# Optimization experiments

Measured on AMD Instinct MI355X. Metric: run time of the kernel, lower is better.

## Reference

```python
import jax, jax.numpy as jnp
import numpy as np

NFFT = 4096
BATCH = 2048
STAGES = 12  # log2(NFFT)


def _bitrev(n):
    bits = int(np.log2(n))
    idx = np.arange(n)
    rev = np.zeros(n, dtype=np.int64)
    for b in range(bits):
        rev |= ((idx >> b) & 1) << (bits - 1 - b)
    return rev


def setup_inputs() -> dict:
    key = jax.random.key(0)
    x = jax.random.normal(key, (BATCH, NFFT), dtype=jnp.float32)
    # bit-reversal permutation matrix, applied as x @ perm -> x[bitrev(k)]
    rev = _bitrev(NFFT)
    perm = np.zeros((NFFT, NFFT), dtype=np.float32)
    perm[rev, np.arange(NFFT)] = 1.0
    # per-stage butterfly weights (real/imag of twiddles), zero-padded to NFFT
    rconvs = np.zeros((STAGES, 2, NFFT), dtype=np.float32)
    iconvs = np.zeros((STAGES, 2, NFFT), dtype=np.float32)
    for i in range(STAGES):
        s = 2 ** (i + 1)
        h = 2 ** i
        th = 2.0 * np.pi * np.arange(h) / s  # twiddle w^j = exp(-i*th)
        c, sn = np.cos(th), np.sin(th)
        rconvs[i, 0, :s] = 1.0
        rconvs[i, 1, :s] = np.concatenate([c, -c])
        iconvs[i, 1, :s] = np.concatenate([-sn, sn])
    return {
        "x": x,
        "perm": jnp.asarray(perm),
        "rconvs": jnp.asarray(rconvs),
        "iconvs": jnp.asarray(iconvs),
    }


def _butterfly(x, w, h):
    # x: [B, M, 2h], w: [2, 2h]; equals the original diag-filter conv1d
    xt, xb = x[..., :h], x[..., h:]
    top = w[0, :h] * xt + w[1, :h] * xb
    bot = w[0, h:] * xt + w[1, h:] * xb
    return jnp.concatenate([top, bot], axis=-1)


def reference(x, perm, rconvs, iconvs):
    B = x.shape[0]
    rx = x @ perm  # bit-reversal reorder (dense matmul as in original)
    ix = jnp.zeros_like(rx)
    for i in range(STAGES):
        s = 2 ** (i + 1)
        h = 2 ** i
        rx = rx.reshape(B, -1, s)
        ix = ix.reshape(B, -1, s)
        rc = rconvs[i, :, :s]
        ic = iconvs[i, :, :s]
        nrx = _butterfly(rx, rc, h) - _butterfly(ix, ic, h)
        nix = _butterfly(ix, rc, h) + _butterfly(rx, ic, h)
        rx = nrx.reshape(B, -1)
        ix = nix.reshape(B, -1)
    return rx.reshape(B, 1, NFFT), ix.reshape(B, 1, NFFT)
```

## Files before the change

### kernel.cpp

```cpp
#include <hip/hip_runtime.h>


constexpr int NFFT  = 4096;
constexpr int BATCH = 2048;
constexpr int RS    = 18;

struct cplx { float re, im; };
__device__ __forceinline__ cplx cmul(cplx a, cplx b){ return {a.re*b.re - a.im*b.im, a.re*b.im + a.im*b.re}; }
__device__ __forceinline__ cplx cadd(cplx a, cplx b){ return {a.re+b.re, a.im+b.im}; }
__device__ __forceinline__ cplx csub(cplx a, cplx b){ return {a.re-b.re, a.im-b.im}; }
__device__ __forceinline__ cplx cnegi(cplx a){ return { a.im, -a.re }; }

__device__ __forceinline__ void dft4(cplx& a, cplx& b, cplx& c, cplx& d){
    cplx t0 = cadd(a,c), t1 = csub(a,c), t2 = cadd(b,d);
    cplx t3n = cnegi(csub(b,d));
    a = cadd(t0,t2);
    cplx nb = cadd(t1,t3n);
    c = csub(t0,t2);
    d = csub(t1,t3n);
    b = nb;
}

__device__ __forceinline__ constexpr int RIDX(int r){ return 4*(r&3) + (r>>2); }

__device__ __forceinline__ void dft16(cplx z[16]){
    dft4(z[0], z[4], z[8],  z[12]);
    dft4(z[1], z[5], z[9],  z[13]);
    dft4(z[2], z[6], z[10], z[14]);
    dft4(z[3], z[7], z[11], z[15]);
    constexpr float C1 = 0.92387953251128675613f;
    constexpr float S1 = 0.38268343236508977173f;
    constexpr float R2 = 0.70710678118654752440f;
    z[5]  = cmul(z[5],  { C1,-S1});
    z[6]  = cmul(z[6],  { R2,-R2});
    z[7]  = cmul(z[7],  { S1,-C1});
    z[9]  = cmul(z[9],  { R2,-R2});
    z[10] = cnegi(z[10]);
    z[11] = cmul(z[11], {-R2,-R2});
    z[13] = cmul(z[13], { S1,-C1});
    z[14] = cmul(z[14], {-R2,-R2});
    z[15] = cmul(z[15], {-C1, S1});
    dft4(z[0],  z[1],  z[2],  z[3]);
    dft4(z[4],  z[5],  z[6],  z[7]);
    dft4(z[8],  z[9],  z[10], z[11]);
    dft4(z[12], z[13], z[14], z[15]);
}

__device__ __forceinline__ void twiddle_all(cplx z[16], float rev){
    float ang = rev * 6.28318530717958647692f;
    float s = __sinf(ang), c = __cosf(ang);
    cplx w[16];
    w[0] = {1.0f, 0.0f};
    w[1] = {c, -s};
#pragma unroll
    for (int r = 2; r < 16; ++r) w[r] = cmul(w[r>>1], w[(r+1)>>1]);
#pragma unroll
    for (int r = 1; r < 16; ++r) z[RIDX(r)] = cmul(z[RIDX(r)], w[r]);
}

__global__ __launch_bounds__(256, 4)
void fft4096_r16(const float* __restrict__ x, float* __restrict__ out) {
    __shared__ float2 su[256 * RS];

    const int row = blockIdx.x;
    const int t   = threadIdx.x;
    const float* __restrict__ xr = x + (size_t)row * NFFT;

    cplx z[16];

#pragma unroll
    for (int n1 = 0; n1 < 16; ++n1) z[n1] = { xr[n1*256 + t], 0.0f };
    dft16(z);
    twiddle_all(z, (float)t * (1.0f/4096.0f));
#pragma unroll
    for (int r = 0; r < 16; ++r) su[t*RS + r] = { z[RIDX(r)].re, z[RIDX(r)].im };

    __syncthreads();

    {
        const int k1 = t >> 4, m2 = t & 15;
#pragma unroll
        for (int m1 = 0; m1 < 16; ++m1) {
            float2 v = su[(16*m1 + m2)*RS + k1];
            z[m1] = { v.x, v.y };
        }
        dft16(z);
        twiddle_all(z, (float)m2 * (1.0f/256.0f));
        __syncthreads();
#pragma unroll
        for (int k2 = 0; k2 < 16; ++k2)
            su[(k1*16 + k2)*RS + m2] = { z[RIDX(k2)].re, z[RIDX(k2)].im };
    }

    __syncthreads();

    {
        const int k1 = t & 15, k2 = t >> 4;
#pragma unroll
        for (int m2 = 0; m2 < 16; ++m2) {
            float2 v = su[(k1*16 + k2)*RS + m2];
            z[m2] = { v.x, v.y };
        }
        dft16(z);
        float* __restrict__ outRe = out + (size_t)row * NFFT;
        float* __restrict__ outIm = out + (size_t)BATCH * NFFT + (size_t)row * NFFT;
#pragma unroll
        for (int k3 = 0; k3 < 16; ++k3) {
            outRe[t + 256*k3] = z[RIDX(k3)].re;
            outIm[t + 256*k3] = z[RIDX(k3)].im;
        }
    }
}

extern "C" void kernel_launch(void* const* d_in, const int* in_sizes, int n_in,
                              void* d_out, int out_size, void* d_ws, size_t ws_size,
                              hipStream_t stream) {
    (void)in_sizes; (void)n_in; (void)d_ws; (void)ws_size; (void)out_size;
    const float* x = (const float*)d_in[0];
    float* out = (float*)d_out;
    fft4096_r16<<<dim3(BATCH), dim3(256), 0, stream>>>(x, out);
}
```

Measured before the change: 132.6 us.

## Pack two real rows into one complex FFT and separate via conjugate symmetry

Result: no change. 135.0 us (+1.8%).

```diff
diff --git a/kernel.cpp b/kernel.cpp
--- a/kernel.cpp
+++ b/kernel.cpp
@@ -59,17 +59,18 @@
 }
 
 __global__ __launch_bounds__(256, 4)
-void fft4096_r16(const float* __restrict__ x, float* __restrict__ out) {
+void fft4096_r16x2(const float* __restrict__ x, float* __restrict__ out) {
     __shared__ float2 su[256 * RS];
 
-    const int row = blockIdx.x;
-    const int t   = threadIdx.x;
-    const float* __restrict__ xr = x + (size_t)row * NFFT;
+    const int pair = blockIdx.x;
+    const int t    = threadIdx.x;
+    const float* __restrict__ xa = x + (size_t)(2*pair) * NFFT;
+    const float* __restrict__ xb = xa + NFFT;
 
     cplx z[16];
 
 #pragma unroll
-    for (int n1 = 0; n1 < 16; ++n1) z[n1] = { xr[n1*256 + t], 0.0f };
+    for (int n1 = 0; n1 < 16; ++n1) z[n1] = { xa[n1*256 + t], xb[n1*256 + t] };
     dft16(z);
     twiddle_all(z, (float)t * (1.0f/4096.0f));
 #pragma unroll
@@ -102,13 +103,29 @@
             z[m2] = { v.x, v.y };
         }
         dft16(z);
-        float* __restrict__ outRe = out + (size_t)row * NFFT;
-        float* __restrict__ outIm = out + (size_t)BATCH * NFFT + (size_t)row * NFFT;
+    }
+
+    __syncthreads();
+
 #pragma unroll
-        for (int k3 = 0; k3 < 16; ++k3) {
-            outRe[t + 256*k3] = z[RIDX(k3)].re;
-            outIm[t + 256*k3] = z[RIDX(k3)].im;
-        }
+    for (int r = 0; r < 16; ++r)
+        su[t + 256*r] = { z[RIDX(r)].re, z[RIDX(r)].im };
+
+    __syncthreads();
+
+    float* __restrict__ outAre = out + (size_t)(2*pair) * NFFT;
+    float* __restrict__ outAim = out + (size_t)BATCH * NFFT + (size_t)(2*pair) * NFFT;
+    float* __restrict__ outBre = outAre + NFFT;
+    float* __restrict__ outBim = outAim + NFFT;
+#pragma unroll
+    for (int r = 0; r < 16; ++r) {
+        const int k = t + 256*r;
+        float2 Zk = su[k];
+        float2 Zm = su[(NFFT - k) & (NFFT - 1)];
+        outAre[k] = 0.5f * (Zk.x + Zm.x);
+        outAim[k] = 0.5f * (Zk.y - Zm.y);
+        outBre[k] = 0.5f * (Zk.y + Zm.y);
+        outBim[k] = 0.5f * (Zm.x - Zk.x);
     }
 }
 
@@ -118,5 +135,5 @@
     (void)in_sizes; (void)n_in; (void)d_ws; (void)ws_size; (void)out_size;
     const float* x = (const float*)d_in[0];
     float* out = (float*)d_out;
-    fft4096_r16<<<dim3(BATCH), dim3(256), 0, stream>>>(x, out);
+    fft4096_r16x2<<<dim3(BATCH / 2), dim3(256), 0, stream>>>(x, out);
 }
```
